# Kernel tuning notes

Measured on AMD Instinct MI355X. Metric: run time of the kernel, lower is better.

## Reference

```python
import jax, jax.numpy as jnp
import numpy as np
import math

NB_BASIS = 100          # add_gaussian_basis_functions
SEQ_SIDE = 14           # 14x14 = 196 image feature grid
RIDGE = 0.5             # ridge_penalty for G = F^T (F F^T + lam I)^-1
BASIS_VAR = 0.001       # sigma = 0.001 * I for every basis Gaussian
TWO_PI = 2.0 * math.pi
EPS_COV = 1e-6          # stabilizer added to fitted covariance


def _positions():
    # compute_positions_efficient: linspace(shift, 1-shift, L0) meshgrid, L0=L1=14
    s = 1.0 / SEQ_SIDE
    lin = np.linspace(s, 1.0 - s, SEQ_SIDE)
    px, py = np.meshgrid(lin, lin, indexing='ij')
    return jnp.asarray(np.stack([px.ravel(), py.ravel()], axis=-1), jnp.float32)  # [L,2]


def _basis_mus():
    # add_gaussian_basis_functions: 10x10 grid of means over [0,1]^2
    lin = np.linspace(0.0, 1.0, int(math.sqrt(NB_BASIS)))
    mx, my = np.meshgrid(lin, lin, indexing='ij')
    return jnp.asarray(np.stack([mx.ravel(), my.ravel()], axis=-1), jnp.float32)  # [N,2]


def _G_matrix(pos, mus):
    # F[j, i] = N(pos_i ; mu_j, BASIS_VAR * I)  (isotropic 2D Gaussian density)
    d2 = jnp.sum((pos[None, :, :] - mus[:, None, :]) ** 2, axis=-1)       # [N,L]
    F = jnp.exp(-0.5 * d2 / BASIS_VAR) / (TWO_PI * BASIS_VAR)
    A = F @ F.T + RIDGE * jnp.eye(NB_BASIS, dtype=F.dtype)                # [N,N]
    return F.T @ jnp.linalg.inv(A)                                        # [L,N]


def setup_inputs() -> dict:
    key = jax.random.key(0)
    ks = jax.random.split(key, 7)
    B, L, H, M, GL, O = 256, 196, 1024, 512, 1, 2048
    x = jax.random.normal(ks[0], (B, L, H), jnp.float32)
    x_mask = jnp.zeros((B, L), dtype=bool)  # True = padded position
    W1 = jax.random.normal(ks[1], (H, M), jnp.float32) * 0.02
    b1 = jnp.zeros((M,), jnp.float32)
    W2 = jax.random.normal(ks[2], (M, GL), jnp.float32) * 0.02
    b2 = jnp.zeros((GL,), jnp.float32)
    Wm = jax.random.normal(ks[3], (H * GL, O), jnp.float32) * 0.02
    bm = jnp.zeros((O,), jnp.float32)
    return {"x": x, "x_mask": x_mask, "W1": W1, "b1": b1,
            "W2": W2, "b2": b2, "Wm": Wm, "bm": bm}


def reference(x, x_mask, W1, b1, W2, b2, Wm, bm):
    # x: [B,L,H] grid features, x_mask: [B,L] bool padding mask
    pos = _positions()            # [L,2]
    mus = _basis_mus()            # [N,2]
    G = _G_matrix(pos, mus)       # [L,N] shared across batch (single length bucket)

    # --- MLP attention (glimpses=1), softmax over sequence dim ---
    logits = jax.nn.relu(x @ W1 + b1) @ W2 + b2          # [B,L,1]
    logits = jnp.where(x_mask[..., None], -1e9, logits)
    att = jax.nn.softmax(logits, axis=1)                 # [B,L,1]
    p = att[..., 0]                                      # [B,L]

    # --- fit 2D Gaussian to attention over positions (continuous softmax params) ---
    mu = p @ pos                                         # [B,2]
    d = pos[None, :, :] - mu[:, None, :]                 # [B,L,2]
    Sigma = jnp.einsum('bl,bli,blj->bij', p, d, d) + EPS_COV * jnp.eye(2, dtype=x.dtype)

    # --- r_j = E_{N(mu,Sigma)}[psi_j] = N(mu_j ; mu, Sigma + BASIS_VAR*I) ---
    S = Sigma + BASIS_VAR * jnp.eye(2, dtype=x.dtype)    # [B,2,2]
    a, b_, c, ddg = S[:, 0, 0], S[:, 0, 1], S[:, 1, 0], S[:, 1, 1]
    det = a * ddg - b_ * c                               # [B]
    Sinv = jnp.stack([jnp.stack([ddg, -b_], -1),
                      jnp.stack([-c, a], -1)], -2) / det[:, None, None]
    dm = mu[:, None, :] - mus[None, :, :]                # [B,N,2]
    quad = jnp.einsum('bni,bij,bnj->bn', dm, Sinv, dm)
    r = jnp.exp(-0.5 * quad) / (TWO_PI * jnp.sqrt(det)[:, None])  # [B,N]

    # --- value_function: B = V^T G; context = B r ---
    Bmat = jnp.einsum('bld,ln->bdn', x, G)               # [B,H,N]
    ctx = jnp.einsum('bdn,bn->bd', Bmat, r)              # [B,H]

    return ctx @ Wm + bm                                 # [B,FLAT_OUT_SIZE]
```

## Files before the change

### kernel.cpp

```cpp
#include <hip/hip_runtime.h>

typedef _Float16 half8v __attribute__((ext_vector_type(8)));
typedef float    f32x4  __attribute__((ext_vector_type(4)));
typedef unsigned short ushort_t;

__device__ __forceinline__ unsigned short f2h(float f) {
  _Float16 h = (_Float16)f;
  return __builtin_bit_cast(unsigned short, h);
}
__device__ __forceinline__ unsigned f2h2(float lo, float hi) {
  return (unsigned)f2h(lo) | ((unsigned)f2h(hi) << 16);
}
__device__ __forceinline__ float lin14(int i) {
  double s = 1.0 / 14.0, stop = 1.0 - s;
  double step = (stop - s) / 13.0;
  return (float)((i == 13) ? stop : s + i * step);
}
__device__ __forceinline__ float lin10(int i) {
  double st = 1.0 / 9.0;
  return (float)((i == 9) ? 1.0 : i * st);
}
__device__ __forceinline__ float wave_sum(float v) {
  #pragma unroll
  for (int o = 32; o; o >>= 1) v += __shfl_xor(v, o, 64);
  return v;
}
__device__ __forceinline__ float wave_max(float v) {
  #pragma unroll
  for (int o = 32; o; o >>= 1) v = fmaxf(v, __shfl_xor(v, o, 64));
  return v;
}
__device__ __forceinline__ float blk_sum(float v, float* red) {
  v = wave_sum(v);
  if ((threadIdx.x & 63) == 0) red[threadIdx.x >> 6] = v;
  __syncthreads();
  v = red[0] + red[1] + red[2] + red[3];
  __syncthreads();
  return v;
}
__device__ __forceinline__ float blk_max(float v, float* red) {
  v = wave_max(v);
  if ((threadIdx.x & 63) == 0) red[threadIdx.x >> 6] = v;
  __syncthreads();
  v = fmaxf(fmaxf(red[0], red[1]), fmaxf(red[2], red[3]));
  __syncthreads();
  return v;
}

__global__ void k_F(float* __restrict__ posg, float* __restrict__ musg,
                    float* __restrict__ Fg) {
  int idx = blockIdx.x * 256 + threadIdx.x;
  if (idx < 196) { posg[2*idx] = lin14(idx / 14); posg[2*idx+1] = lin14(idx % 14); }
  if (idx < 100) { musg[2*idx] = lin10(idx / 10); musg[2*idx+1] = lin10(idx % 10); }
  if (idx < 19600) {
    int k = idx / 196, l = idx % 196;
    float mx = lin10(k / 10), my = lin10(k % 10);
    float px = lin14(l / 14), py = lin14(l % 14);
    double dx = (double)mx - (double)px, dy = (double)my - (double)py;
    double d2 = dx * dx + dy * dy;
    Fg[idx] = (float)(exp(-500.0 * d2) / (6.283185307179586 * 0.001));
  }
}

__global__ void k_A(const float* __restrict__ Fg, double* __restrict__ A) {
  int i = blockIdx.x, j = threadIdx.x;
  if (j < 100) {
    const float* Fi = Fg + i * 196;
    const float* Fj = Fg + j * 196;
    double s = 0.0;
    for (int l = 0; l < 196; ++l) s += (double)Fi[l] * (double)Fj[l];
    if (i == j) s += 0.5;
    A[i * 100 + j] = s;
  }
}

__global__ __launch_bounds__(512) void k_inv(const double* __restrict__ Ag,
                                             double* __restrict__ Ainv) {
  __shared__ double rowraw[100], colraw[100], rkv[100], ckv[100];
  int t = threadIdx.x;
  int rb = t / 20, cb = t % 20;
  bool own = t < 500;
  double a[4][5];
  if (own) {
    #pragma unroll
    for (int r = 0; r < 4; ++r)
      #pragma unroll
      for (int c = 0; c < 5; ++c)
        a[r][c] = Ag[(4 * rb + r) * 100 + 5 * cb + c];
  }
  __syncthreads();
  for (int k = 0; k < 100; ++k) {
    int krb = k >> 2, klr = k & 3;
    int kcb = k / 5,  klc = k - 5 * kcb;
    if (own && rb == krb) {
      #pragma unroll
      for (int r = 0; r < 4; ++r)
        if (r == klr) {
          #pragma unroll
          for (int c = 0; c < 5; ++c) rowraw[5 * cb + c] = a[r][c];
        }
    }
    if (own && cb == kcb) {
      #pragma unroll
      for (int c = 0; c < 5; ++c)
        if (c == klc) {
          #pragma unroll
          for (int r = 0; r < 4; ++r) colraw[4 * rb + r] = a[r][c];
        }
    }
    __syncthreads();
    if (t < 100) {
      double p = rowraw[k], pinv = 1.0 / p;
      rkv[t] = (t == k) ? 1.0 + pinv : rowraw[t] * pinv;
      ckv[t] = (t == k) ? p - 1.0    : colraw[t];
    }
    __syncthreads();
    if (own) {
      double ckl[4], rkl[5];
      #pragma unroll
      for (int r = 0; r < 4; ++r) ckl[r] = ckv[4 * rb + r];
      #pragma unroll
      for (int c = 0; c < 5; ++c) rkl[c] = rkv[5 * cb + c];
      #pragma unroll
      for (int r = 0; r < 4; ++r)
        #pragma unroll
        for (int c = 0; c < 5; ++c)
          a[r][c] = fma(-ckl[r], rkl[c], a[r][c]);
    }
  }
  if (own) {
    #pragma unroll
    for (int r = 0; r < 4; ++r)
      #pragma unroll
      for (int c = 0; c < 5; ++c)
        Ainv[(4 * rb + r) * 100 + 5 * cb + c] = a[r][c];
  }
}

__global__ void k_G(const float* __restrict__ Fg, const double* __restrict__ Ainv,
                    float* __restrict__ G) {
  int l = blockIdx.x, n = threadIdx.x;
  if (n < 100) {
    double s = 0.0;
    for (int k = 0; k < 100; ++k) s += (double)Fg[k * 196 + l] * Ainv[k * 100 + n];
    G[l * 100 + n] = (float)s;
  }
}

__global__ void k_splitw1(const float* __restrict__ W1, ushort_t* __restrict__ W1t) {
  __shared__ float t[32][33];
  int n0 = blockIdx.x * 32, k0 = blockIdx.y * 32;
  int tx = threadIdx.x, ty = threadIdx.y;
  #pragma unroll
  for (int i = 0; i < 32; i += 8)
    t[ty + i][tx] = W1[(size_t)(k0 + ty + i) * 512 + n0 + tx];
  __syncthreads();
  #pragma unroll
  for (int i = 0; i < 32; i += 8)
    W1t[(size_t)(n0 + ty + i) * 1024 + k0 + tx] = f2h(t[tx][ty + i]);
}

__global__ void k_wmT(const float* __restrict__ Wm, ushort_t* __restrict__ WmT) {
  __shared__ float t[32][33];
  int n0 = blockIdx.x * 32, k0 = blockIdx.y * 32;
  int tx = threadIdx.x, ty = threadIdx.y;
  #pragma unroll
  for (int i = 0; i < 32; i += 8)
    t[ty + i][tx] = Wm[(size_t)(k0 + ty + i) * 2048 + n0 + tx];
  __syncthreads();
  #pragma unroll
  for (int i = 0; i < 32; i += 8)
    WmT[(size_t)(n0 + ty + i) * 1024 + k0 + tx] = f2h(t[tx][ty + i]);
}

__global__ __launch_bounds__(256, 2) void k_gemm1(
    const float* __restrict__ x, const ushort_t* __restrict__ W1t,
    const float* __restrict__ b1, const float* __restrict__ W2,
    float* __restrict__ logits) {
  __shared__ __align__(16) ushort_t As[2][128 * 40];
  __shared__ __align__(16) ushort_t Bs[2][128 * 40];

  int bid  = blockIdx.x;
  int bid2 = (bid & 7) * 196 + (bid >> 3);
  int tm = bid2 >> 2, tn = bid2 & 3;
  size_t row0 = (size_t)tm * 128;
  int n0 = tn * 128;
  int tid = threadIdx.x, lane = tid & 63;
  int wid = tid >> 6, wm = wid >> 1, wn = wid & 1;

  const float*    xp = x   + (row0 + (tid >> 3)) * 1024 + ((tid & 7) << 2);
  const ushort_t* wp = W1t + (size_t)(n0 + (tid >> 2)) * 1024 + ((tid & 3) << 3);
  int so_a = (tid >> 3) * 40 + ((tid & 7) << 2);
  int so_b = (tid >> 2) * 40 + ((tid & 3) << 3);

  int aro = (wm * 64 + (lane & 15)) * 40 + ((lane >> 4) << 3);
  int bro = (wn * 64 + (lane & 15)) * 40 + ((lane >> 4) << 3);

  f32x4 acc[4][4] = {};
  float4 a4[4]; uint4 b4[2];

  #pragma unroll
  for (int r = 0; r < 4; ++r) a4[r] = *(const float4*)(xp + r * 32 * 1024);
  #pragma unroll
  for (int r = 0; r < 2; ++r) b4[r] = *(const uint4*)(wp + r * 64 * 1024);
  #pragma unroll
  for (int r = 0; r < 4; ++r) {
    uint2 w; w.x = f2h2(a4[r].x, a4[r].y); w.y = f2h2(a4[r].z, a4[r].w);
    *(uint2*)&As[0][so_a + r * 32 * 40] = w;
  }
  #pragma unroll
  for (int r = 0; r < 2; ++r) *(uint4*)&Bs[0][so_b + r * 64 * 40] = b4[r];
  __syncthreads();

  int cur = 0;
  for (int ks = 0; ks < 32; ++ks) {
    if (ks < 31) {
      #pragma unroll
      for (int r = 0; r < 4; ++r)
        a4[r] = *(const float4*)(xp + (ks + 1) * 32 + r * 32 * 1024);
      #pragma unroll
      for (int r = 0; r < 2; ++r)
        b4[r] = *(const uint4*)(wp + (ks + 1) * 32 + r * 64 * 1024);
    }
    half8v af[4], bf[4];
    #pragma unroll
    for (int i = 0; i < 4; ++i) af[i] = *(const half8v*)&As[cur][aro + i * 16 * 40];
    #pragma unroll
    for (int i = 0; i < 4; ++i) bf[i] = *(const half8v*)&Bs[cur][bro + i * 16 * 40];
    #pragma unroll
    for (int i = 0; i < 4; ++i)
      #pragma unroll
      for (int j = 0; j < 4; ++j)
        acc[i][j] = __builtin_amdgcn_mfma_f32_16x16x32_f16(af[i], bf[j], acc[i][j], 0, 0, 0);
    if (ks < 31) {
      #pragma unroll
      for (int r = 0; r < 4; ++r) {
        uint2 w; w.x = f2h2(a4[r].x, a4[r].y); w.y = f2h2(a4[r].z, a4[r].w);
        *(uint2*)&As[cur ^ 1][so_a + r * 32 * 40] = w;
      }
      #pragma unroll
      for (int r = 0; r < 2; ++r) *(uint4*)&Bs[cur ^ 1][so_b + r * 64 * 40] = b4[r];
    }
    __syncthreads();
    cur ^= 1;
  }

  int cbase = n0 + wn * 64 + (lane & 15);
  float b1v[4], w2v[4];
  #pragma unroll
  for (int j = 0; j < 4; ++j) { b1v[j] = b1[cbase + j * 16]; w2v[j] = W2[cbase + j * 16]; }
  float part[4][4];
  #pragma unroll
  for (int i = 0; i < 4; ++i)
    #pragma unroll
    for (int q = 0; q < 4; ++q) {
      float s = 0.f;
      #pragma unroll
      for (int j = 0; j < 4; ++j) {
        float h = acc[i][j][q] + b1v[j];
        s += fmaxf(h, 0.f) * w2v[j];
      }
      part[i][q] = s;
    }
  #pragma unroll
  for (int off = 1; off < 16; off <<= 1)
    #pragma unroll
    for (int i = 0; i < 4; ++i)
      #pragma unroll
      for (int q = 0; q < 4; ++q)
        part[i][q] += __shfl_xor(part[i][q], off, 64);
  if ((lane & 15) == 0) {
    int rbase = (int)row0 + wm * 64 + ((lane >> 4) << 2);
    #pragma unroll
    for (int i = 0; i < 4; ++i)
      #pragma unroll
      for (int q = 0; q < 4; ++q)
        atomicAdd(&logits[rbase + i * 16 + q], part[i][q]);
  }
}

__global__ __launch_bounds__(256) void k_batch(
    const float* __restrict__ logits, const unsigned char* __restrict__ mask,
    const float* __restrict__ b2, const float* __restrict__ pos,
    const float* __restrict__ mus, const float* __restrict__ G,
    float* __restrict__ g_out) {
  __shared__ float red[4];
  __shared__ float rsh[100];
  int b = blockIdx.x, tid = threadIdx.x;
  bool act = tid < 196;
  float lg = -1e30f;
  if (act) {
    lg = logits[b * 196 + tid] + b2[0];
    if (mask[b * 196 + tid]) lg = -1e9f;
  }
  float m = blk_max(lg, red);
  float e = act ? expf(lg - m) : 0.f;
  float Z = blk_sum(e, red);
  float pv = e / Z;
  float px = act ? pos[2 * tid] : 0.f, py = act ? pos[2 * tid + 1] : 0.f;
  float mux = blk_sum(pv * px, red);
  float muy = blk_sum(pv * py, red);
  float dx = px - mux, dy = py - muy;
  float sxx = blk_sum(pv * dx * dx, red);
  float sxy = blk_sum(pv * dx * dy, red);
  float syy = blk_sum(pv * dy * dy, red);
  float aa = (sxx + 1e-6f) + 1e-3f;
  float bb = sxy;
  float dd = (syy + 1e-6f) + 1e-3f;
  float det = aa * dd - bb * bb;
  float scale = 1.f / (6.2831853071795864f * sqrtf(det));
  if (tid < 100) {
    float dmx = mux - mus[2 * tid], dmy = muy - mus[2 * tid + 1];
    float quad = (dd * dmx * dmx - 2.f * bb * dmx * dmy + aa * dmy * dmy) / det;
    rsh[tid] = expf(-0.5f * quad) * scale;
  }
  __syncthreads();
  if (act) {
    const float* Gr = G + tid * 100;
    float s = 0.f;
    #pragma unroll 4
    for (int n = 0; n < 100; ++n) s = fmaf(Gr[n], rsh[n], s);
    g_out[b * 196 + tid] = s;
  }
}

__global__ __launch_bounds__(256) void k_ctx(const float* __restrict__ x,
                                             const float* __restrict__ g,
                                             ushort_t* __restrict__ ctxh) {
  int b = blockIdx.y, seg = blockIdx.x, tid = threadIdx.x;
  __shared__ float gs[196];
  if (tid < 196) gs[tid] = g[b * 196 + tid];
  __syncthreads();
  int d = seg * 256 + tid;
  const float* xp = x + (size_t)b * 200704 + d;
  float acc = 0.f;
  #pragma unroll 8
  for (int l = 0; l < 196; ++l) acc = fmaf(xp[(size_t)l * 1024], gs[l], acc);
  ctxh[b * 1024 + d] = f2h(acc);
}

__global__ __launch_bounds__(256, 2) void k_out2(
    const ushort_t* __restrict__ ctxh, const ushort_t* __restrict__ WmT,
    const float* __restrict__ bm, float* __restrict__ out) {
  __shared__ __align__(16) ushort_t As[2][64 * 40];
  __shared__ __align__(16) ushort_t Bs[2][128 * 40];
  int n0 = blockIdx.x * 128;
  int m0 = blockIdx.y * 64;
  int tid = threadIdx.x, lane = tid & 63;
  int wid = tid >> 6, wm = wid >> 1, wn = wid & 1;

  int arow = tid >> 2, aseg = (tid & 3) << 3;
  const ushort_t* ap = ctxh + (m0 + arow) * 1024 + aseg;
  int aso = arow * 40 + aseg;
  int brow = tid >> 1, bsh = (tid & 1) << 4;
  const ushort_t* bp = WmT + (size_t)(n0 + brow) * 1024 + bsh;
  int bso = brow * 40 + bsh;

  int aro = (wm * 32 + (lane & 15)) * 40 + ((lane >> 4) << 3);
  int bro = (wn * 64 + (lane & 15)) * 40 + ((lane >> 4) << 3);

  f32x4 acc[2][4] = {};
  uint4 a4, b4[2];
  a4 = *(const uint4*)ap;
  b4[0] = *(const uint4*)bp; b4[1] = *(const uint4*)(bp + 8);
  *(uint4*)&As[0][aso] = a4;
  *(uint4*)&Bs[0][bso] = b4[0]; *(uint4*)&Bs[0][bso + 8] = b4[1];
  __syncthreads();

  int cur = 0;
  for (int ks = 0; ks < 32; ++ks) {
    if (ks < 31) {
      a4 = *(const uint4*)(ap + (ks + 1) * 32);
      b4[0] = *(const uint4*)(bp + (ks + 1) * 32);
      b4[1] = *(const uint4*)(bp + (ks + 1) * 32 + 8);
    }
    half8v af[2], bf[4];
    #pragma unroll
    for (int i = 0; i < 2; ++i) af[i] = *(const half8v*)&As[cur][aro + i * 16 * 40];
    #pragma unroll
    for (int j = 0; j < 4; ++j) bf[j] = *(const half8v*)&Bs[cur][bro + j * 16 * 40];
    #pragma unroll
    for (int i = 0; i < 2; ++i)
      #pragma unroll
      for (int j = 0; j < 4; ++j)
        acc[i][j] = __builtin_amdgcn_mfma_f32_16x16x32_f16(af[i], bf[j], acc[i][j], 0, 0, 0);
    if (ks < 31) {
      *(uint4*)&As[cur ^ 1][aso] = a4;
      *(uint4*)&Bs[cur ^ 1][bso] = b4[0]; *(uint4*)&Bs[cur ^ 1][bso + 8] = b4[1];
    }
    __syncthreads();
    cur ^= 1;
  }

  int rbase = m0 + wm * 32 + ((lane >> 4) << 2);
  int cbase = n0 + wn * 64 + (lane & 15);
  #pragma unroll
  for (int j = 0; j < 4; ++j) {
    float bmv = bm[cbase + j * 16];
    #pragma unroll
    for (int i = 0; i < 2; ++i)
      #pragma unroll
      for (int q = 0; q < 4; ++q)
        out[(size_t)(rbase + i * 16 + q) * 2048 + cbase + j * 16] = acc[i][j][q] + bmv;
  }
}

extern "C" void kernel_launch(void* const* d_in, const int* in_sizes, int n_in,
                              void* d_out, int out_size, void* d_ws, size_t ws_size,
                              hipStream_t stream) {
  const float* x  = (const float*)d_in[0];
  const unsigned char* xmask = (const unsigned char*)d_in[1];
  const float* W1 = (const float*)d_in[2];
  const float* b1 = (const float*)d_in[3];
  const float* W2 = (const float*)d_in[4];
  const float* b2 = (const float*)d_in[5];
  const float* Wm = (const float*)d_in[6];
  const float* bm = (const float*)d_in[7];
  float* out = (float*)d_out;

  char* ws = (char*)d_ws;
  float*    Fg     = (float*)(ws + 0);
  double*   Ainv   = (double*)(ws + 78400);
  double*   Atmp   = (double*)(ws + 158400);
  float*    posg   = (float*)(ws + 238400);
  float*    musg   = (float*)(ws + 239968);
  float*    G      = (float*)(ws + 240768);
  float*    logits = (float*)(ws + 319168);
  float*    gbuf   = (float*)(ws + 519872);
  ushort_t* ctxh   = (ushort_t*)(ws + 720576);
  ushort_t* W1t    = (ushort_t*)(ws + 1244864);
  ushort_t* WmT    = (ushort_t*)(ws + 2293440);

  k_F<<<77, 256, 0, stream>>>(posg, musg, Fg);
  k_A<<<100, 128, 0, stream>>>(Fg, Atmp);
  k_inv<<<1, 512, 0, stream>>>(Atmp, Ainv);
  k_G<<<196, 128, 0, stream>>>(Fg, Ainv, G);
  k_splitw1<<<dim3(16, 32), dim3(32, 8), 0, stream>>>(W1, W1t);
  k_wmT<<<dim3(64, 32), dim3(32, 8), 0, stream>>>(Wm, WmT);
  hipMemsetAsync(logits, 0, 200704, stream);
  k_gemm1<<<1568, 256, 0, stream>>>(x, W1t, b1, W2, logits);
  k_batch<<<256, 256, 0, stream>>>(logits, xmask, b2, posg, musg, G, gbuf);
  k_ctx<<<dim3(4, 256), 256, 0, stream>>>(x, gbuf, ctxh);
  k_out2<<<dim3(16, 4), 256, 0, stream>>>(ctxh, WmT, bm, out);
}
```

Before: 524.1 us.

## Deepen GEMM1 global prefetch to two stages, transpose G, halve inverse threads

```diff
diff --git a/kernel.cpp b/kernel.cpp
--- a/kernel.cpp
+++ b/kernel.cpp
@@ -74,35 +74,35 @@
   }
 }
 
-__global__ __launch_bounds__(512) void k_inv(const double* __restrict__ Ag,
+__global__ __launch_bounds__(256) void k_inv(const double* __restrict__ Ag,
                                              double* __restrict__ Ainv) {
   __shared__ double rowraw[100], colraw[100], rkv[100], ckv[100];
   int t = threadIdx.x;
-  int rb = t / 20, cb = t % 20;
-  bool own = t < 500;
-  double a[4][5];
+  int rb = t / 10, cb = t % 10;
+  bool own = t < 250;
+  double a[4][10];
   if (own) {
     #pragma unroll
     for (int r = 0; r < 4; ++r)
       #pragma unroll
-      for (int c = 0; c < 5; ++c)
-        a[r][c] = Ag[(4 * rb + r) * 100 + 5 * cb + c];
+      for (int c = 0; c < 10; ++c)
+        a[r][c] = Ag[(4 * rb + r) * 100 + 10 * cb + c];
   }
   __syncthreads();
   for (int k = 0; k < 100; ++k) {
     int krb = k >> 2, klr = k & 3;
-    int kcb = k / 5,  klc = k - 5 * kcb;
+    int kcb = k / 10, klc = k - 10 * kcb;
     if (own && rb == krb) {
       #pragma unroll
       for (int r = 0; r < 4; ++r)
         if (r == klr) {
           #pragma unroll
-          for (int c = 0; c < 5; ++c) rowraw[5 * cb + c] = a[r][c];
+          for (int c = 0; c < 10; ++c) rowraw[10 * cb + c] = a[r][c];
         }
     }
     if (own && cb == kcb) {
       #pragma unroll
-      for (int c = 0; c < 5; ++c)
+      for (int c = 0; c < 10; ++c)
         if (c == klc) {
           #pragma unroll
           for (int r = 0; r < 4; ++r) colraw[4 * rb + r] = a[r][c];
@@ -116,15 +116,15 @@
     }
     __syncthreads();
     if (own) {
-      double ckl[4], rkl[5];
+      double ckl[4], rkl[10];
       #pragma unroll
       for (int r = 0; r < 4; ++r) ckl[r] = ckv[4 * rb + r];
       #pragma unroll
-      for (int c = 0; c < 5; ++c) rkl[c] = rkv[5 * cb + c];
+      for (int c = 0; c < 10; ++c) rkl[c] = rkv[10 * cb + c];
       #pragma unroll
       for (int r = 0; r < 4; ++r)
         #pragma unroll
-        for (int c = 0; c < 5; ++c)
+        for (int c = 0; c < 10; ++c)
           a[r][c] = fma(-ckl[r], rkl[c], a[r][c]);
     }
   }
@@ -132,18 +132,18 @@
     #pragma unroll
     for (int r = 0; r < 4; ++r)
       #pragma unroll
-      for (int c = 0; c < 5; ++c)
-        Ainv[(4 * rb + r) * 100 + 5 * cb + c] = a[r][c];
+      for (int c = 0; c < 10; ++c)
+        Ainv[(4 * rb + r) * 100 + 10 * cb + c] = a[r][c];
   }
 }
 
 __global__ void k_G(const float* __restrict__ Fg, const double* __restrict__ Ainv,
-                    float* __restrict__ G) {
+                    float* __restrict__ Gt) {
   int l = blockIdx.x, n = threadIdx.x;
   if (n < 100) {
     double s = 0.0;
     for (int k = 0; k < 100; ++k) s += (double)Fg[k * 196 + l] * Ainv[k * 100 + n];
-    G[l * 100 + n] = (float)s;
+    Gt[n * 196 + l] = (float)s;
   }
 }
 
@@ -188,61 +188,82 @@
   int tid = threadIdx.x, lane = tid & 63;
   int wid = tid >> 6, wm = wid >> 1, wn = wid & 1;
 
-  const float*    xp = x   + (row0 + (tid >> 3)) * 1024 + ((tid & 7) << 2);
+  const float*    xp = x   + (row0 + (tid >> 2)) * 1024 + ((tid & 3) << 3);
   const ushort_t* wp = W1t + (size_t)(n0 + (tid >> 2)) * 1024 + ((tid & 3) << 3);
-  int so_a = (tid >> 3) * 40 + ((tid & 7) << 2);
-  int so_b = (tid >> 2) * 40 + ((tid & 3) << 3);
+  int so = (tid >> 2) * 40 + ((tid & 3) << 3);
 
   int aro = (wm * 64 + (lane & 15)) * 40 + ((lane >> 4) << 3);
   int bro = (wn * 64 + (lane & 15)) * 40 + ((lane >> 4) << 3);
 
   f32x4 acc[4][4] = {};
-  float4 a4[4]; uint4 b4[2];
-
-  #pragma unroll
-  for (int r = 0; r < 4; ++r) a4[r] = *(const float4*)(xp + r * 32 * 1024);
-  #pragma unroll
-  for (int r = 0; r < 2; ++r) b4[r] = *(const uint4*)(wp + r * 64 * 1024);
-  #pragma unroll
-  for (int r = 0; r < 4; ++r) {
-    uint2 w; w.x = f2h2(a4[r].x, a4[r].y); w.y = f2h2(a4[r].z, a4[r].w);
-    *(uint2*)&As[0][so_a + r * 32 * 40] = w;
-  }
-  #pragma unroll
-  for (int r = 0; r < 2; ++r) *(uint4*)&Bs[0][so_b + r * 64 * 40] = b4[r];
-  __syncthreads();
-
-  int cur = 0;
-  for (int ks = 0; ks < 32; ++ks) {
-    if (ks < 31) {
-      #pragma unroll
-      for (int r = 0; r < 4; ++r)
-        a4[r] = *(const float4*)(xp + (ks + 1) * 32 + r * 32 * 1024);
-      #pragma unroll
-      for (int r = 0; r < 2; ++r)
-        b4[r] = *(const uint4*)(wp + (ks + 1) * 32 + r * 64 * 1024);
-    }
+
+  float4 aP[4], aQ[4]; uint4 bP[2], bQ[2];
+
+  auto issueP = [&](int ks) {
+    #pragma unroll
+    for (int r = 0; r < 2; ++r) {
+      aP[2*r]   = *(const float4*)(xp + ks * 32 + r * 64 * 1024);
+      aP[2*r+1] = *(const float4*)(xp + ks * 32 + r * 64 * 1024 + 4);
+      bP[r]     = *(const uint4*)(wp + ks * 32 + r * 64 * 1024);
+    }
+  };
+  auto issueQ = [&](int ks) {
+    #pragma unroll
+    for (int r = 0; r < 2; ++r) {
+      aQ[2*r]   = *(const float4*)(xp + ks * 32 + r * 64 * 1024);
+      aQ[2*r+1] = *(const float4*)(xp + ks * 32 + r * 64 * 1024 + 4);
+      bQ[r]     = *(const uint4*)(wp + ks * 32 + r * 64 * 1024);
+    }
+  };
+  auto writeP = [&](int buf) {
+    #pragma unroll
+    for (int r = 0; r < 2; ++r) {
+      uint4 w;
+      w.x = f2h2(aP[2*r].x, aP[2*r].y);   w.y = f2h2(aP[2*r].z, aP[2*r].w);
+      w.z = f2h2(aP[2*r+1].x, aP[2*r+1].y); w.w = f2h2(aP[2*r+1].z, aP[2*r+1].w);
+      *(uint4*)&As[buf][so + r * 64 * 40] = w;
+      *(uint4*)&Bs[buf][so + r * 64 * 40] = bP[r];
+    }
+  };
+  auto writeQ = [&](int buf) {
+    #pragma unroll
+    for (int r = 0; r < 2; ++r) {
+      uint4 w;
+      w.x = f2h2(aQ[2*r].x, aQ[2*r].y);   w.y = f2h2(aQ[2*r].z, aQ[2*r].w);
+      w.z = f2h2(aQ[2*r+1].x, aQ[2*r+1].y); w.w = f2h2(aQ[2*r+1].z, aQ[2*r+1].w);
+      *(uint4*)&As[buf][so + r * 64 * 40] = w;
+      *(uint4*)&Bs[buf][so + r * 64 * 40] = bQ[r];
+    }
+  };
+  auto mmac = [&](int buf) {
     half8v af[4], bf[4];
     #pragma unroll
-    for (int i = 0; i < 4; ++i) af[i] = *(const half8v*)&As[cur][aro + i * 16 * 40];
-    #pragma unroll
-    for (int i = 0; i < 4; ++i) bf[i] = *(const half8v*)&Bs[cur][bro + i * 16 * 40];
+    for (int i = 0; i < 4; ++i) af[i] = *(const half8v*)&As[buf][aro + i * 16 * 40];
+    #pragma unroll
+    for (int i = 0; i < 4; ++i) bf[i] = *(const half8v*)&Bs[buf][bro + i * 16 * 40];
     #pragma unroll
     for (int i = 0; i < 4; ++i)
       #pragma unroll
       for (int j = 0; j < 4; ++j)
         acc[i][j] = __builtin_amdgcn_mfma_f32_16x16x32_f16(af[i], bf[j], acc[i][j], 0, 0, 0);
-    if (ks < 31) {
-      #pragma unroll
-      for (int r = 0; r < 4; ++r) {
-        uint2 w; w.x = f2h2(a4[r].x, a4[r].y); w.y = f2h2(a4[r].z, a4[r].w);
-        *(uint2*)&As[cur ^ 1][so_a + r * 32 * 40] = w;
-      }
-      #pragma unroll
-      for (int r = 0; r < 2; ++r) *(uint4*)&Bs[cur ^ 1][so_b + r * 64 * 40] = b4[r];
-    }
+  };
+
+  issueP(0);
+  writeP(0);
+  issueQ(1);
+  __syncthreads();
+
+  #pragma unroll 1
+  for (int kp = 0; kp < 16; ++kp) {
+    int e = 2 * kp;
+    if (e < 30) issueP(e + 2);
+    mmac(0);
+    if (e < 31) writeQ(1);
     __syncthreads();
-    cur ^= 1;
+    if (e + 1 < 30) issueQ(e + 3);
+    mmac(1);
+    if (e + 1 < 31) writeP(0);
+    __syncthreads();
   }
 
   int cbase = n0 + wn * 64 + (lane & 15);
@@ -282,7 +303,7 @@
 __global__ __launch_bounds__(256) void k_batch(
     const float* __restrict__ logits, const unsigned char* __restrict__ mask,
     const float* __restrict__ b2, const float* __restrict__ pos,
-    const float* __restrict__ mus, const float* __restrict__ G,
+    const float* __restrict__ mus, const float* __restrict__ Gt,
     float* __restrict__ g_out) {
   __shared__ float red[4];
   __shared__ float rsh[100];
@@ -316,10 +337,9 @@
   }
   __syncthreads();
   if (act) {
-    const float* Gr = G + tid * 100;
     float s = 0.f;
     #pragma unroll 4
-    for (int n = 0; n < 100; ++n) s = fmaf(Gr[n], rsh[n], s);
+    for (int n = 0; n < 100; ++n) s = fmaf(Gt[n * 196 + tid], rsh[n], s);
     g_out[b * 196 + tid] = s;
   }
 }
@@ -424,7 +444,7 @@
   double*   Atmp   = (double*)(ws + 158400);
   float*    posg   = (float*)(ws + 238400);
   float*    musg   = (float*)(ws + 239968);
-  float*    G      = (float*)(ws + 240768);
+  float*    Gt     = (float*)(ws + 240768);
   float*    logits = (float*)(ws + 319168);
   float*    gbuf   = (float*)(ws + 519872);
   ushort_t* ctxh   = (ushort_t*)(ws + 720576);
@@ -433,13 +453,13 @@
 
   k_F<<<77, 256, 0, stream>>>(posg, musg, Fg);
   k_A<<<100, 128, 0, stream>>>(Fg, Atmp);
-  k_inv<<<1, 512, 0, stream>>>(Atmp, Ainv);
-  k_G<<<196, 128, 0, stream>>>(Fg, Ainv, G);
+  k_inv<<<1, 256, 0, stream>>>(Atmp, Ainv);
+  k_G<<<196, 128, 0, stream>>>(Fg, Ainv, Gt);
   k_splitw1<<<dim3(16, 32), dim3(32, 8), 0, stream>>>(W1, W1t);
   k_wmT<<<dim3(64, 32), dim3(32, 8), 0, stream>>>(Wm, WmT);
   hipMemsetAsync(logits, 0, 200704, stream);
   k_gemm1<<<1568, 256, 0, stream>>>(x, W1t, b1, W2, logits);
-  k_batch<<<256, 256, 0, stream>>>(logits, xmask, b2, posg, musg, G, gbuf);
+  k_batch<<<256, 256, 0, stream>>>(logits, xmask, b2, posg, musg, Gt, gbuf);
   k_ctx<<<dim3(4, 256), 256, 0, stream>>>(x, gbuf, ctxh);
   k_out2<<<dim3(16, 4), 256, 0, stream>>>(ctxh, WmT, bm, out);
 }
```

New measurement: 623.4 us. 18.9% more time.
